# Performance work log

Hardware: AMD Instinct MI355X
Metric: run time of the kernel (lower is better)

## Reference

```python
import jax, jax.numpy as jnp
import numpy as np
from jax import lax

B, T, V, D, K = 64, 512, 32000, 768, 29

def setup_inputs() -> dict:
    key = jax.random.key(0)
    ks = jax.random.split(key, 8)
    x = jax.random.randint(ks[0], (B, T), 0, V)
    tags = jax.random.randint(ks[1], (B, T), 0, K)
    emb = jax.random.normal(ks[2], (V, D), dtype=jnp.float32) * 0.02
    w = jax.random.normal(ks[3], (K, D), dtype=jnp.float32) * 0.02
    b = jnp.zeros((K,), dtype=jnp.float32)
    start_trans = jax.random.normal(ks[4], (K,), dtype=jnp.float32) * 0.1
    end_trans = jax.random.normal(ks[5], (K,), dtype=jnp.float32) * 0.1
    trans = jax.random.normal(ks[6], (K, K), dtype=jnp.float32) * 0.1
    return {"x": x, "tags": tags, "emb": emb, "w": w, "b": b,
            "start_trans": start_trans, "end_trans": end_trans, "trans": trans}

def _emissions(x, emb, w, b):
    e = emb[x]                                   # [B,T,D] (dropout is identity at inference)
    return jnp.einsum('btd,kd->btk', e, w) + b   # [B,T,K]

def _crf_nll(em, tags, start_trans, end_trans, trans):
    # numerator: score of the gold tag path (full mask)
    num = start_trans[tags[:, 0]]
    num = num + jnp.take_along_axis(em[:, 0], tags[:, 0:1], axis=1)[:, 0]
    num = num + jnp.sum(trans[tags[:, :-1], tags[:, 1:]], axis=1)
    num = num + jnp.sum(jnp.take_along_axis(em[:, 1:], tags[:, 1:, None], axis=2)[..., 0], axis=1)
    num = num + end_trans[tags[:, -1]]
    # denominator: forward algorithm (log partition)
    def step(alpha, e_t):
        # alpha [B,K] prev-tag scores; e_t [B,K] current emissions
        nxt = jax.nn.logsumexp(alpha[:, :, None] + trans[None], axis=1) + e_t
        return nxt, None
    alpha0 = start_trans[None] + em[:, 0]
    alpha, _ = lax.scan(step, alpha0, jnp.swapaxes(em[:, 1:], 0, 1))
    logZ = jax.nn.logsumexp(alpha + end_trans[None], axis=1)
    return -jnp.sum(num - logZ)  # torchcrf default reduction='sum', model negates

def _viterbi(em, start_trans, end_trans, trans):
    def vstep(score, e_t):
        cand = score[:, :, None] + trans[None]   # [B,K_prev,K_cur]
        bp = jnp.argmax(cand, axis=1)            # [B,K]
        return jnp.max(cand, axis=1) + e_t, bp
    score0 = start_trans[None] + em[:, 0]
    score, bps = lax.scan(vstep, score0, jnp.swapaxes(em[:, 1:], 0, 1))  # bps [T-1,B,K]
    last = jnp.argmax(score + end_trans[None], axis=1)                   # [B]
    def back(tag, bp):
        prev = jnp.take_along_axis(bp, tag[:, None], axis=1)[:, 0]
        return prev, prev
    _, path = lax.scan(back, last, bps, reverse=True)                    # [T-1,B], tags 0..T-2
    return jnp.concatenate([jnp.swapaxes(path, 0, 1), last[:, None]], axis=1)

def reference(x, tags, emb, w, b, start_trans, end_trans, trans):
    em = _emissions(x, emb, w, b)
    nll = _crf_nll(em, tags, start_trans, end_trans, trans)
    decoded = _viterbi(em, start_trans, end_trans, trans)
    return nll, decoded
```

## Files before the change

kernel.cpp:

```cpp
#include <hip/hip_runtime.h>
#include <math.h>

#define NB 64
#define NT 512
#define ND 768
#define NK 29
#define L2E 1.4426950408889634f
#define LN2 0.6931471805599453f
#define NEG_BIG -1e30f

typedef __attribute__((ext_vector_type(8))) short short8;
typedef __attribute__((ext_vector_type(4))) float floatx4;

__device__ __forceinline__ short bf16r(float f) {
    unsigned u = __float_as_uint(f);
    unsigned r = (u + 0x7FFFu + ((u >> 16) & 1u)) >> 16;
    return (short)r;
}

__device__ __forceinline__ float rlane(float v, int i) {
    return __int_as_float(__builtin_amdgcn_readlane(__float_as_int(v), i));
}

__global__ __launch_bounds__(256) void k_prep(const float* __restrict__ w,
                                              short* __restrict__ wbf)
{
    int i = blockIdx.x * 256 + threadIdx.x;
    if (i < 32 * ND) {
        int row = i / ND;
        wbf[i] = (row < NK) ? bf16r(w[i]) : (short)0;
    }
}

__global__ __launch_bounds__(128) void k_emissions(
    const int* __restrict__ x, const float* __restrict__ emb,
    const short* __restrict__ wbf, const float* __restrict__ bias,
    float* __restrict__ em)
{
    __shared__ float red[2 * 256];
    const int lane = threadIdx.x & 63;
    const int wv = threadIdx.x >> 6;
    const int col = lane & 15;
    const int quad = lane >> 4;
    const int Mbase = blockIdx.x * 16;
    const int tok = Mbase + col;

    const float* arow = emb + (size_t)x[tok] * ND + wv * 384 + quad * 8;
    const short* brow0 = wbf + (size_t)col * ND + wv * 384 + quad * 8;
    const short* brow1 = brow0 + 16 * ND;

    float4 a[24];
#pragma unroll
    for (int c = 0; c < 12; ++c) {
        a[2 * c]     = *(const float4*)(arow + c * 32);
        a[2 * c + 1] = *(const float4*)(arow + c * 32 + 4);
    }

    floatx4 acc0 = {0.f, 0.f, 0.f, 0.f};
    floatx4 acc1 = {0.f, 0.f, 0.f, 0.f};

    short8 b0 = *(const short8*)(brow0);
    short8 b1 = *(const short8*)(brow1);

#pragma unroll
    for (int c = 0; c < 12; ++c) {
        int c1 = (c + 1 <= 11) ? c + 1 : 11;
        short8 nb0 = *(const short8*)(brow0 + c1 * 32);
        short8 nb1 = *(const short8*)(brow1 + c1 * 32);

        short8 af;
        af[0] = bf16r(a[2 * c].x);     af[1] = bf16r(a[2 * c].y);
        af[2] = bf16r(a[2 * c].z);     af[3] = bf16r(a[2 * c].w);
        af[4] = bf16r(a[2 * c + 1].x); af[5] = bf16r(a[2 * c + 1].y);
        af[6] = bf16r(a[2 * c + 1].z); af[7] = bf16r(a[2 * c + 1].w);

        acc0 = __builtin_amdgcn_mfma_f32_16x16x32_bf16(af, b0, acc0, 0, 0, 0);
        acc1 = __builtin_amdgcn_mfma_f32_16x16x32_bf16(af, b1, acc1, 0, 0, 0);

        b0 = nb0; b1 = nb1;
    }

    const int r0 = quad * 4;
    if (wv == 1) {
#pragma unroll
        for (int reg = 0; reg < 4; ++reg) {
            red[(r0 + reg) * 16 + col]       = acc0[reg];
            red[256 + (r0 + reg) * 16 + col] = acc1[reg];
        }
    }
    __syncthreads();
    if (wv == 0) {
        float bs0 = bias[col];
        float bs1 = (col < NK - 16) ? bias[16 + col] : 0.f;
#pragma unroll
        for (int reg = 0; reg < 4; ++reg) {
            int row = r0 + reg;
            float v0 = acc0[reg] + red[row * 16 + col] + bs0;
            em[(size_t)(Mbase + row) * NK + col] = v0;
            if (col < NK - 16) {
                float v1 = acc1[reg] + red[256 + row * 16 + col] + bs1;
                em[(size_t)(Mbase + row) * NK + 16 + col] = v1;
            }
        }
    }
}

__global__ __launch_bounds__(64) void k_scan(
    const float* __restrict__ em, const int* __restrict__ tags,
    const float* __restrict__ st, const float* __restrict__ en,
    const float* __restrict__ tr, float* __restrict__ part,
    float* __restrict__ out)
{
    __shared__ __align__(16) unsigned char smem[NT * NK * 4];
    const int lane = threadIdx.x;
    const int c = lane & 31;
    const int jc = (c < NK) ? c : NK - 1;

    if (blockIdx.x < NB) {
        const int b = blockIdx.x;
        float* emS = (float*)smem;
        {
            const float4* src = (const float4*)(em + (size_t)b * NT * NK);
            float4* dst = (float4*)emS;
            for (int i = lane; i < NT * NK / 4; i += 64) dst[i] = src[i];
        }
        float EC[32];
#pragma unroll
        for (int i = 0; i < NK; ++i) EC[i] = __expf(tr[i * NK + jc]);
#pragma unroll
        for (int i = NK; i < 32; ++i) EC[i] = 0.f;

        float anew = __expf(st[jc] + emS[jc]);

        int eshift = 5 * (NT - 1);
        float eemc = exp2f(fmaf(emS[NK + jc], L2E, -5.0f));
        float rawn = emS[2 * NK + jc];

        for (int t = 1; t < NT; ++t) {
            float curm = (c < NK) ? anew : 0.f;
            float S[32];
#pragma unroll
            for (int i = 0; i < 32; ++i) S[i] = rlane(curm, i);
            float p0 = 0.f, p1 = 0.f, p2 = 0.f, p3 = 0.f;
#pragma unroll
            for (int ii = 0; ii < 8; ++ii) {
                p0 = fmaf(S[4 * ii + 0], EC[4 * ii + 0], p0);
                p1 = fmaf(S[4 * ii + 1], EC[4 * ii + 1], p1);
                p2 = fmaf(S[4 * ii + 2], EC[4 * ii + 2], p2);
                p3 = fmaf(S[4 * ii + 3], EC[4 * ii + 3], p3);
            }
            anew = ((p0 + p1) + (p2 + p3)) * eemc;
            eemc = exp2f(fmaf(rawn, L2E, -5.0f));
            int tn = t + 2; tn = tn < NT ? tn : NT - 1;
            rawn = emS[tn * NK + jc];

            if ((t & 15) == 0) {
                unsigned mb = (unsigned)__builtin_amdgcn_readfirstlane(
                                  __float_as_int(anew));
                int ex = (int)((mb >> 23) & 255u) - 127;
                anew *= __int_as_float((unsigned)(127 - ex) << 23);
                eshift += ex;
            }
        }
        float val = (lane < NK) ? anew * __expf(en[jc]) : 0.f;
#pragma unroll
        for (int s = 32; s; s >>= 1) val += __shfl_xor(val, s);
        float logZ = logf(val) + (float)eshift * LN2;
        const int* tg = tags + b * NT;
        float p = 0.f;
        for (int t = lane; t < NT; t += 64) {
            int tt = tg[t];
            p += emS[t * NK + tt];
            if (t == 0) p += st[tt];
            else        p += tr[tg[t - 1] * NK + tt];
            if (t == NT - 1) p += en[tt];
        }
#pragma unroll
        for (int s = 32; s; s >>= 1) p += __shfl_xor(p, s);
        if (lane == 0) part[b] = logZ - p;
    } else {
        const int b = blockIdx.x - NB;
        const float* emb_b = em + (size_t)b * NT * NK;
        unsigned char* sbp = smem;
        unsigned char* smap = smem + 511 * 32;

        float Tc[32];
#pragma unroll
        for (int i = 0; i < NK; ++i) Tc[i] = tr[i * NK + jc];
#pragma unroll
        for (int i = NK; i < 32; ++i) Tc[i] = 0.f;

        float sc = (c < NK) ? (st[jc] + emb_b[jc]) : NEG_BIG;

        float e0 = emb_b[1 * NK + jc];
        float e1 = emb_b[2 * NK + jc];
        float e2 = emb_b[3 * NK + jc];
        float e3 = emb_b[4 * NK + jc];

        auto vstep = [&](int t, float emt) {
            float S[32];
#pragma unroll
            for (int i = 0; i < 32; ++i) S[i] = rlane(sc, i);
            float v[32]; int id[32];
#pragma unroll
            for (int i = 0; i < 32; ++i) { v[i] = S[i] + Tc[i]; id[i] = i; }
#pragma unroll
            for (int w2 = 16; w2 >= 1; w2 >>= 1)
#pragma unroll
                for (int i = 0; i < 16; ++i) {
                    if (i < w2) {
                        bool g = v[i + w2] > v[i];
                        v[i] = g ? v[i + w2] : v[i];
                        id[i] = g ? id[i + w2] : id[i];
                    }
                }
            if (lane < 32) sbp[(t - 1) * 32 + lane] = (unsigned char)id[0];
            sc = (c < NK) ? (v[0] + emt) : NEG_BIG;
        };

        int t = 1;
        for (; t + 3 < NT; t += 4) {
            vstep(t + 0, e0); { int tn = t + 4; tn = tn < NT ? tn : NT - 1; e0 = emb_b[tn * NK + jc]; }
            vstep(t + 1, e1); { int tn = t + 5; tn = tn < NT ? tn : NT - 1; e1 = emb_b[tn * NK + jc]; }
            vstep(t + 2, e2); { int tn = t + 6; tn = tn < NT ? tn : NT - 1; e2 = emb_b[tn * NK + jc]; }
            vstep(t + 3, e3); { int tn = t + 7; tn = tn < NT ? tn : NT - 1; e3 = emb_b[tn * NK + jc]; }
        }
        vstep(509, e0); vstep(510, e1); vstep(511, e2);

        float vfin = (lane < NK) ? (sc + en[jc]) : NEG_BIG;
        float M = vfin;
#pragma unroll
        for (int s = 32; s; s >>= 1) M = fmaxf(M, __shfl_xor(M, s));
        unsigned long long mk = __ballot((lane < NK) && vfin == M);
        int last = (int)__builtin_ctzll(mk);

        const int h = lane >> 5;
        int cur8[8];
#pragma unroll
        for (int rep = 0; rep < 8; ++rep) cur8[rep] = c;
        for (int off = 0; off < 32; ++off) {
#pragma unroll
            for (int rep = 0; rep < 8; ++rep) {
                int s = 2 * rep + h;
                int hi = (s == 15) ? 511 : 32 * s + 32;
                int r = hi - 1 - off;
                if (r >= 32 * s) cur8[rep] = sbp[r * 32 + cur8[rep]];
            }
        }
#pragma unroll
        for (int rep = 0; rep < 8; ++rep)
            smap[(2 * rep + h) * 32 + c] = (unsigned char)cur8[rep];

        int myhi = 0, cur = last;
        for (int s = 15; s >= 0; --s) {
            if (lane == s) myhi = cur;
            cur = smap[s * 32 + cur];
        }
        float* op = out + 1 + (size_t)b * NT;
        if (lane == 16) op[NT - 1] = (float)last;
        if (lane < 16) {
            int s = lane;
            int hi = (s == 15) ? 511 : 32 * s + 32;
            int cc = myhi;
            for (int r = hi - 1; r >= 32 * s; --r) {
                cc = sbp[r * 32 + cc];
                op[r] = (float)cc;
            }
        }
    }
}

__global__ __launch_bounds__(64) void k_finish(const float* __restrict__ part,
                                               float* __restrict__ out)
{
    float v = part[threadIdx.x];
#pragma unroll
    for (int s = 32; s; s >>= 1) v += __shfl_xor(v, s);
    if (threadIdx.x == 0) out[0] = v;
}

extern "C" void kernel_launch(void* const* d_in, const int* in_sizes, int n_in,
                              void* d_out, int out_size, void* d_ws, size_t ws_size,
                              hipStream_t stream) {
    const int*   x    = (const int*)d_in[0];
    const int*   tags = (const int*)d_in[1];
    const float* emb  = (const float*)d_in[2];
    const float* w    = (const float*)d_in[3];
    const float* bias = (const float*)d_in[4];
    const float* st   = (const float*)d_in[5];
    const float* en   = (const float*)d_in[6];
    const float* tr   = (const float*)d_in[7];
    float* out = (float*)d_out;

    short* wbf  = (short*)d_ws;
    float* part = (float*)((char*)d_ws + 49152);
    float* em   = (float*)((char*)d_ws + 65536);

    k_prep<<<96, 256, 0, stream>>>(w, wbf);
    k_emissions<<<2048, 128, 0, stream>>>(x, emb, wbf, bias, em);
    k_scan<<<2 * NB, 64, 0, stream>>>(em, tags, st, en, tr, part, out);
    k_finish<<<1, 64, 0, stream>>>(part, out);
}
```

Before: 343.1 us.

## Interleave multiple sequences per wavefront in CRF forward and Viterbi scans

Each forward-algorithm wavefront now handles four batch sequences and each Viterbi wavefront handles two, interleaving their independent recurrences so their latency chains overlap. The per-step broadcast of the state vector moves from 32 readlane ops to an LDS store followed by float4 LDS loads. Emissions are read straight from global memory instead of being staged into LDS first. In exchange, fewer blocks are launched (48 instead of 128), each running a longer serial loop, which lowers parallelism across the GPU.

```diff
diff --git a/kernel.cpp b/kernel.cpp
--- a/kernel.cpp
+++ b/kernel.cpp
@@ -5,6 +5,7 @@
 #define NT 512
 #define ND 768
 #define NK 29
+#define NCRF 16
 #define L2E 1.4426950408889634f
 #define LN2 0.6931471805599453f
 #define NEG_BIG -1e30f
@@ -16,10 +17,6 @@
     unsigned u = __float_as_uint(f);
     unsigned r = (u + 0x7FFFu + ((u >> 16) & 1u)) >> 16;
     return (short)r;
-}
-
-__device__ __forceinline__ float rlane(float v, int i) {
-    return __int_as_float(__builtin_amdgcn_readlane(__float_as_int(v), i));
 }
 
 __global__ __launch_bounds__(256) void k_prep(const float* __restrict__ w,
@@ -111,18 +108,19 @@
     const float* __restrict__ tr, float* __restrict__ part,
     float* __restrict__ out)
 {
-    __shared__ __align__(16) unsigned char smem[NT * NK * 4];
+    __shared__ __align__(16) float sAll[4 * 32];
+    __shared__ __align__(16) unsigned char smem[2 * 511 * 32 + 512];
     const int lane = threadIdx.x;
-    const int c = lane & 31;
-    const int jc = (c < NK) ? c : NK - 1;
-
-    if (blockIdx.x < NB) {
-        const int b = blockIdx.x;
-        float* emS = (float*)smem;
-        {
-            const float4* src = (const float4*)(em + (size_t)b * NT * NK);
-            float4* dst = (float4*)emS;
-            for (int i = lane; i < NT * NK / 4; i += 64) dst[i] = src[i];
+    const int jc = (lane < NK) ? lane : NK - 1;
+
+    if (blockIdx.x < NCRF) {
+        const int bI = blockIdx.x;
+        const float* emk[4];
+        const int* tgk[4];
+#pragma unroll
+        for (int k = 0; k < 4; ++k) {
+            emk[k] = em + (size_t)(4 * bI + k) * NT * NK;
+            tgk[k] = tags + (size_t)(4 * bI + k) * NT;
         }
         float EC[32];
 #pragma unroll
@@ -130,59 +128,87 @@
 #pragma unroll
         for (int i = NK; i < 32; ++i) EC[i] = 0.f;
 
-        float anew = __expf(st[jc] + emS[jc]);
-
-        int eshift = 5 * (NT - 1);
-        float eemc = exp2f(fmaf(emS[NK + jc], L2E, -5.0f));
-        float rawn = emS[2 * NK + jc];
+        float anew[4], eemc[4], rawn[4];
+        int eshift[4];
+#pragma unroll
+        for (int k = 0; k < 4; ++k) {
+            anew[k] = __expf(st[jc] + emk[k][jc]);
+            if (lane < 32) sAll[32 * k + lane] = (lane < NK) ? anew[k] : 0.f;
+            eshift[k] = 5 * (NT - 1);
+            eemc[k] = exp2f(fmaf(emk[k][NK + jc], L2E, -5.0f));
+            rawn[k] = emk[k][2 * NK + jc];
+        }
 
         for (int t = 1; t < NT; ++t) {
-            float curm = (c < NK) ? anew : 0.f;
-            float S[32];
-#pragma unroll
-            for (int i = 0; i < 32; ++i) S[i] = rlane(curm, i);
-            float p0 = 0.f, p1 = 0.f, p2 = 0.f, p3 = 0.f;
-#pragma unroll
-            for (int ii = 0; ii < 8; ++ii) {
-                p0 = fmaf(S[4 * ii + 0], EC[4 * ii + 0], p0);
-                p1 = fmaf(S[4 * ii + 1], EC[4 * ii + 1], p1);
-                p2 = fmaf(S[4 * ii + 2], EC[4 * ii + 2], p2);
-                p3 = fmaf(S[4 * ii + 3], EC[4 * ii + 3], p3);
-            }
-            anew = ((p0 + p1) + (p2 + p3)) * eemc;
-            eemc = exp2f(fmaf(rawn, L2E, -5.0f));
-            int tn = t + 2; tn = tn < NT ? tn : NT - 1;
-            rawn = emS[tn * NK + jc];
-
+#pragma unroll
+            for (int k = 0; k < 4; ++k) {
+                const float4* sA4 = (const float4*)(sAll + 32 * k);
+                float4 A[8];
+#pragma unroll
+                for (int ii = 0; ii < 8; ++ii) A[ii] = sA4[ii];
+                float p0 = 0.f, p1 = 0.f, p2 = 0.f, p3 = 0.f;
+#pragma unroll
+                for (int ii = 0; ii < 8; ++ii) {
+                    p0 = fmaf(A[ii].x, EC[4 * ii + 0], p0);
+                    p1 = fmaf(A[ii].y, EC[4 * ii + 1], p1);
+                    p2 = fmaf(A[ii].z, EC[4 * ii + 2], p2);
+                    p3 = fmaf(A[ii].w, EC[4 * ii + 3], p3);
+                }
+                anew[k] = ((p0 + p1) + (p2 + p3)) * eemc[k];
+                eemc[k] = exp2f(fmaf(rawn[k], L2E, -5.0f));
+                int tn = t + 2; tn = tn < NT ? tn : NT - 1;
+                rawn[k] = emk[k][tn * NK + jc];
+            }
             if ((t & 15) == 0) {
-                unsigned mb = (unsigned)__builtin_amdgcn_readfirstlane(
-                                  __float_as_int(anew));
-                int ex = (int)((mb >> 23) & 255u) - 127;
-                anew *= __int_as_float((unsigned)(127 - ex) << 23);
-                eshift += ex;
-            }
-        }
-        float val = (lane < NK) ? anew * __expf(en[jc]) : 0.f;
-#pragma unroll
-        for (int s = 32; s; s >>= 1) val += __shfl_xor(val, s);
-        float logZ = logf(val) + (float)eshift * LN2;
-        const int* tg = tags + b * NT;
-        float p = 0.f;
-        for (int t = lane; t < NT; t += 64) {
-            int tt = tg[t];
-            p += emS[t * NK + tt];
-            if (t == 0) p += st[tt];
-            else        p += tr[tg[t - 1] * NK + tt];
-            if (t == NT - 1) p += en[tt];
-        }
-#pragma unroll
-        for (int s = 32; s; s >>= 1) p += __shfl_xor(p, s);
-        if (lane == 0) part[b] = logZ - p;
+#pragma unroll
+                for (int k = 0; k < 4; ++k) {
+                    unsigned mb = (unsigned)__builtin_amdgcn_readfirstlane(
+                                      __float_as_int(anew[k]));
+                    int ex = (int)((mb >> 23) & 255u) - 127;
+                    anew[k] *= __int_as_float((unsigned)(127 - ex) << 23);
+                    eshift[k] += ex;
+                }
+            }
+#pragma unroll
+            for (int k = 0; k < 4; ++k)
+                if (lane < 32) sAll[32 * k + lane] = (lane < NK) ? anew[k] : 0.f;
+        }
+
+        float pp[4] = {0.f, 0.f, 0.f, 0.f};
+#pragma unroll
+        for (int it = 0; it < 8; ++it) {
+            int t = lane + 64 * it;
+#pragma unroll
+            for (int k = 0; k < 4; ++k) {
+                int tt = tgk[k][t];
+                pp[k] += emk[k][t * NK + tt];
+                if (t == 0) pp[k] += st[tt];
+                else        pp[k] += tr[tgk[k][t - 1] * NK + tt];
+                if (t == NT - 1) pp[k] += en[tt];
+            }
+        }
+#pragma unroll
+        for (int k = 0; k < 4; ++k) {
+            float val = (lane < NK) ? anew[k] * __expf(en[jc]) : 0.f;
+#pragma unroll
+            for (int s = 32; s; s >>= 1) val += __shfl_xor(val, s);
+            float logZ = logf(val) + (float)eshift[k] * LN2;
+            float p = pp[k];
+#pragma unroll
+            for (int s = 32; s; s >>= 1) p += __shfl_xor(p, s);
+            if (lane == 0) part[4 * bI + k] = logZ - p;
+        }
     } else {
-        const int b = blockIdx.x - NB;
-        const float* emb_b = em + (size_t)b * NT * NK;
-        unsigned char* sbp = smem;
-        unsigned char* smap = smem + 511 * 32;
+        const int b0 = 2 * (blockIdx.x - NCRF);
+        const float* emA = em + (size_t)b0 * NT * NK;
+        const float* emB = emA + NT * NK;
+        unsigned char* sbpA = smem;
+        unsigned char* sbpB = smem + 511 * 32;
+        unsigned char* smap = smem + 2 * 511 * 32;
+        float* sA_A = sAll;
+        float* sA_B = sAll + 32;
+        const float4* sA_A4 = (const float4*)sA_A;
+        const float4* sA_B4 = (const float4*)sA_B;
 
         float Tc[32];
 #pragma unroll
@@ -190,81 +216,141 @@
 #pragma unroll
         for (int i = NK; i < 32; ++i) Tc[i] = 0.f;
 
-        float sc = (c < NK) ? (st[jc] + emb_b[jc]) : NEG_BIG;
-
-        float e0 = emb_b[1 * NK + jc];
-        float e1 = emb_b[2 * NK + jc];
-        float e2 = emb_b[3 * NK + jc];
-        float e3 = emb_b[4 * NK + jc];
-
-        auto vstep = [&](int t, float emt) {
-            float S[32];
-#pragma unroll
-            for (int i = 0; i < 32; ++i) S[i] = rlane(sc, i);
-            float v[32]; int id[32];
-#pragma unroll
-            for (int i = 0; i < 32; ++i) { v[i] = S[i] + Tc[i]; id[i] = i; }
-#pragma unroll
-            for (int w2 = 16; w2 >= 1; w2 >>= 1)
-#pragma unroll
-                for (int i = 0; i < 16; ++i) {
-                    if (i < w2) {
+        float scA = (lane < NK) ? (st[jc] + emA[jc]) : NEG_BIG;
+        float scB = (lane < NK) ? (st[jc] + emB[jc]) : NEG_BIG;
+        if (lane < 32) {
+            sA_A[lane] = (lane < NK) ? scA : NEG_BIG;
+            sA_B[lane] = (lane < NK) ? scB : NEG_BIG;
+        }
+
+        float eA0 = emA[1 * NK + jc], eA1 = emA[2 * NK + jc];
+        float eA2 = emA[3 * NK + jc], eA3 = emA[4 * NK + jc];
+        float eB0 = emB[1 * NK + jc], eB1 = emB[2 * NK + jc];
+        float eB2 = emB[3 * NK + jc], eB3 = emB[4 * NK + jc];
+
+        auto vstep2 = [&](int t, float emtA, float emtB) {
+            float4 qA[8], qB[8];
+#pragma unroll
+            for (int ii = 0; ii < 8; ++ii) qA[ii] = sA_A4[ii];
+#pragma unroll
+            for (int ii = 0; ii < 8; ++ii) qB[ii] = sA_B4[ii];
+            {
+                float v[32]; int id[32];
+#pragma unroll
+                for (int ii = 0; ii < 8; ++ii) {
+                    v[4 * ii + 0] = qA[ii].x + Tc[4 * ii + 0];
+                    v[4 * ii + 1] = qA[ii].y + Tc[4 * ii + 1];
+                    v[4 * ii + 2] = qA[ii].z + Tc[4 * ii + 2];
+                    v[4 * ii + 3] = qA[ii].w + Tc[4 * ii + 3];
+                }
+#pragma unroll
+                for (int i = 0; i < 32; ++i) id[i] = i;
+#pragma unroll
+                for (int w2 = 16; w2 >= 1; w2 >>= 1)
+#pragma unroll
+                    for (int i = 0; i < 16; ++i) if (i < w2) {
                         bool g = v[i + w2] > v[i];
                         v[i] = g ? v[i + w2] : v[i];
                         id[i] = g ? id[i + w2] : id[i];
                     }
-                }
-            if (lane < 32) sbp[(t - 1) * 32 + lane] = (unsigned char)id[0];
-            sc = (c < NK) ? (v[0] + emt) : NEG_BIG;
+                if (lane < 32) sbpA[(t - 1) * 32 + lane] = (unsigned char)id[0];
+                scA = (lane < NK) ? (v[0] + emtA) : NEG_BIG;
+                if (lane < 32) sA_A[lane] = (lane < NK) ? scA : NEG_BIG;
+            }
+            {
+                float v[32]; int id[32];
+#pragma unroll
+                for (int ii = 0; ii < 8; ++ii) {
+                    v[4 * ii + 0] = qB[ii].x + Tc[4 * ii + 0];
+                    v[4 * ii + 1] = qB[ii].y + Tc[4 * ii + 1];
+                    v[4 * ii + 2] = qB[ii].z + Tc[4 * ii + 2];
+                    v[4 * ii + 3] = qB[ii].w + Tc[4 * ii + 3];
+                }
+#pragma unroll
+                for (int i = 0; i < 32; ++i) id[i] = i;
+#pragma unroll
+                for (int w2 = 16; w2 >= 1; w2 >>= 1)
+#pragma unroll
+                    for (int i = 0; i < 16; ++i) if (i < w2) {
+                        bool g = v[i + w2] > v[i];
+                        v[i] = g ? v[i + w2] : v[i];
+                        id[i] = g ? id[i + w2] : id[i];
+                    }
+                if (lane < 32) sbpB[(t - 1) * 32 + lane] = (unsigned char)id[0];
+                scB = (lane < NK) ? (v[0] + emtB) : NEG_BIG;
+                if (lane < 32) sA_B[lane] = (lane < NK) ? scB : NEG_BIG;
+            }
         };
 
         int t = 1;
         for (; t + 3 < NT; t += 4) {
-            vstep(t + 0, e0); { int tn = t + 4; tn = tn < NT ? tn : NT - 1; e0 = emb_b[tn * NK + jc]; }
-            vstep(t + 1, e1); { int tn = t + 5; tn = tn < NT ? tn : NT - 1; e1 = emb_b[tn * NK + jc]; }
-            vstep(t + 2, e2); { int tn = t + 6; tn = tn < NT ? tn : NT - 1; e2 = emb_b[tn * NK + jc]; }
-            vstep(t + 3, e3); { int tn = t + 7; tn = tn < NT ? tn : NT - 1; e3 = emb_b[tn * NK + jc]; }
-        }
-        vstep(509, e0); vstep(510, e1); vstep(511, e2);
-
-        float vfin = (lane < NK) ? (sc + en[jc]) : NEG_BIG;
-        float M = vfin;
-#pragma unroll
-        for (int s = 32; s; s >>= 1) M = fmaxf(M, __shfl_xor(M, s));
-        unsigned long long mk = __ballot((lane < NK) && vfin == M);
-        int last = (int)__builtin_ctzll(mk);
-
+            vstep2(t + 0, eA0, eB0);
+            { int tn = t + 4; tn = tn < NT ? tn : NT - 1;
+              eA0 = emA[tn * NK + jc]; eB0 = emB[tn * NK + jc]; }
+            vstep2(t + 1, eA1, eB1);
+            { int tn = t + 5; tn = tn < NT ? tn : NT - 1;
+              eA1 = emA[tn * NK + jc]; eB1 = emB[tn * NK + jc]; }
+            vstep2(t + 2, eA2, eB2);
+            { int tn = t + 6; tn = tn < NT ? tn : NT - 1;
+              eA2 = emA[tn * NK + jc]; eB2 = emB[tn * NK + jc]; }
+            vstep2(t + 3, eA3, eB3);
+            { int tn = t + 7; tn = tn < NT ? tn : NT - 1;
+              eA3 = emA[tn * NK + jc]; eB3 = emB[tn * NK + jc]; }
+        }
+        vstep2(509, eA0, eB0); vstep2(510, eA1, eB1); vstep2(511, eA2, eB2);
+
+        float vfA = (lane < NK) ? (scA + en[jc]) : NEG_BIG;
+        float MA = vfA;
+#pragma unroll
+        for (int s = 32; s; s >>= 1) MA = fmaxf(MA, __shfl_xor(MA, s));
+        unsigned long long mkA = __ballot((lane < NK) && vfA == MA);
+        int lastA = (int)__builtin_ctzll(mkA);
+
+        float vfB = (lane < NK) ? (scB + en[jc]) : NEG_BIG;
+        float MB = vfB;
+#pragma unroll
+        for (int s = 32; s; s >>= 1) MB = fmaxf(MB, __shfl_xor(MB, s));
+        unsigned long long mkB = __ballot((lane < NK) && vfB == MB);
+        int lastB = (int)__builtin_ctzll(mkB);
+
+        const int c = lane & 31;
         const int h = lane >> 5;
-        int cur8[8];
-#pragma unroll
-        for (int rep = 0; rep < 8; ++rep) cur8[rep] = c;
-        for (int off = 0; off < 32; ++off) {
-#pragma unroll
-            for (int rep = 0; rep < 8; ++rep) {
-                int s = 2 * rep + h;
+#pragma unroll
+        for (int chain = 0; chain < 2; ++chain) {
+            const unsigned char* sbp = chain ? sbpB : sbpA;
+            int last = chain ? lastB : lastA;
+            float* op = out + 1 + (size_t)(b0 + chain) * NT;
+
+            int cur8[8];
+#pragma unroll
+            for (int rep = 0; rep < 8; ++rep) cur8[rep] = c;
+            for (int off = 0; off < 32; ++off) {
+#pragma unroll
+                for (int rep = 0; rep < 8; ++rep) {
+                    int s = 2 * rep + h;
+                    int hi = (s == 15) ? 511 : 32 * s + 32;
+                    int r = hi - 1 - off;
+                    if (r >= 32 * s) cur8[rep] = sbp[r * 32 + cur8[rep]];
+                }
+            }
+#pragma unroll
+            for (int rep = 0; rep < 8; ++rep)
+                smap[(2 * rep + h) * 32 + c] = (unsigned char)cur8[rep];
+
+            int myhi = 0, cur = last;
+            for (int s = 15; s >= 0; --s) {
+                if (lane == s) myhi = cur;
+                cur = smap[s * 32 + cur];
+            }
+            if (lane == 16) op[NT - 1] = (float)last;
+            if (lane < 16) {
+                int s = lane;
                 int hi = (s == 15) ? 511 : 32 * s + 32;
-                int r = hi - 1 - off;
-                if (r >= 32 * s) cur8[rep] = sbp[r * 32 + cur8[rep]];
-            }
-        }
-#pragma unroll
-        for (int rep = 0; rep < 8; ++rep)
-            smap[(2 * rep + h) * 32 + c] = (unsigned char)cur8[rep];
-
-        int myhi = 0, cur = last;
-        for (int s = 15; s >= 0; --s) {
-            if (lane == s) myhi = cur;
-            cur = smap[s * 32 + cur];
-        }
-        float* op = out + 1 + (size_t)b * NT;
-        if (lane == 16) op[NT - 1] = (float)last;
-        if (lane < 16) {
-            int s = lane;
-            int hi = (s == 15) ? 511 : 32 * s + 32;
-            int cc = myhi;
-            for (int r = hi - 1; r >= 32 * s; --r) {
-                cc = sbp[r * 32 + cc];
-                op[r] = (float)cc;
+                int cc = myhi;
+                for (int r = hi - 1; r >= 32 * s; --r) {
+                    cc = sbp[r * 32 + cc];
+                    op[r] = (float)cc;
+                }
             }
         }
     }
@@ -298,6 +384,6 @@
 
     k_prep<<<96, 256, 0, stream>>>(w, wbf);
     k_emissions<<<2048, 128, 0, stream>>>(x, emb, wbf, bias, em);
-    k_scan<<<2 * NB, 64, 0, stream>>>(em, tags, st, en, tr, part, out);
+    k_scan<<<NCRF + NB / 2, 64, 0, stream>>>(em, tags, st, en, tr, part, out);
     k_finish<<<1, 64, 0, stream>>>(part, out);
 }
```

After: 567.5 us. 65.4% more time.

## Split Viterbi argmax out of serial scan into parallel backpointer kernel

Applied to the files above, without the earlier changes.

The serial Viterbi scan now does only a max reduction per step and writes every step's score vector to global memory. A new kernel with 512 threads per batch row recomputes the argmax backpointers for all time steps in parallel from the stored scores, then runs the backtrace. Both scans also broadcast state through shared memory with float4 reads instead of 32 readlanes. This takes the argmax index tracking off the serial dependency chain, at the cost of an extra launch, global traffic for the states, and per-step LDS round trips in a single wave.

```diff
diff --git a/kernel.cpp b/kernel.cpp
--- a/kernel.cpp
+++ b/kernel.cpp
@@ -18,10 +18,6 @@
     return (short)r;
 }
 
-__device__ __forceinline__ float rlane(float v, int i) {
-    return __int_as_float(__builtin_amdgcn_readlane(__float_as_int(v), i));
-}
-
 __global__ __launch_bounds__(256) void k_prep(const float* __restrict__ w,
                                               short* __restrict__ wbf)
 {
@@ -109,12 +105,13 @@
     const float* __restrict__ em, const int* __restrict__ tags,
     const float* __restrict__ st, const float* __restrict__ en,
     const float* __restrict__ tr, float* __restrict__ part,
-    float* __restrict__ out)
-{
+    float* __restrict__ states)
+{
+    __shared__ __align__(16) float sA[32];
     __shared__ __align__(16) unsigned char smem[NT * NK * 4];
+    const float4* sA4 = (const float4*)sA;
     const int lane = threadIdx.x;
-    const int c = lane & 31;
-    const int jc = (c < NK) ? c : NK - 1;
+    const int jc = (lane < NK) ? lane : NK - 1;
 
     if (blockIdx.x < NB) {
         const int b = blockIdx.x;
@@ -130,24 +127,25 @@
 #pragma unroll
         for (int i = NK; i < 32; ++i) EC[i] = 0.f;
 
-        float anew = __expf(st[jc] + emS[jc]);
+        float a0v = __expf(st[jc] + emS[jc]);
+        if (lane < 32) sA[lane] = (lane < NK) ? a0v : 0.f;
 
         int eshift = 5 * (NT - 1);
         float eemc = exp2f(fmaf(emS[NK + jc], L2E, -5.0f));
         float rawn = emS[2 * NK + jc];
+        float anew = a0v;
 
         for (int t = 1; t < NT; ++t) {
-            float curm = (c < NK) ? anew : 0.f;
-            float S[32];
-#pragma unroll
-            for (int i = 0; i < 32; ++i) S[i] = rlane(curm, i);
+            float4 A[8];
+#pragma unroll
+            for (int ii = 0; ii < 8; ++ii) A[ii] = sA4[ii];
             float p0 = 0.f, p1 = 0.f, p2 = 0.f, p3 = 0.f;
 #pragma unroll
             for (int ii = 0; ii < 8; ++ii) {
-                p0 = fmaf(S[4 * ii + 0], EC[4 * ii + 0], p0);
-                p1 = fmaf(S[4 * ii + 1], EC[4 * ii + 1], p1);
-                p2 = fmaf(S[4 * ii + 2], EC[4 * ii + 2], p2);
-                p3 = fmaf(S[4 * ii + 3], EC[4 * ii + 3], p3);
+                p0 = fmaf(A[ii].x, EC[4 * ii + 0], p0);
+                p1 = fmaf(A[ii].y, EC[4 * ii + 1], p1);
+                p2 = fmaf(A[ii].z, EC[4 * ii + 2], p2);
+                p3 = fmaf(A[ii].w, EC[4 * ii + 3], p3);
             }
             anew = ((p0 + p1) + (p2 + p3)) * eemc;
             eemc = exp2f(fmaf(rawn, L2E, -5.0f));
@@ -161,6 +159,7 @@
                 anew *= __int_as_float((unsigned)(127 - ex) << 23);
                 eshift += ex;
             }
+            if (lane < 32) sA[lane] = (lane < NK) ? anew : 0.f;
         }
         float val = (lane < NK) ? anew * __expf(en[jc]) : 0.f;
 #pragma unroll
@@ -181,8 +180,7 @@
     } else {
         const int b = blockIdx.x - NB;
         const float* emb_b = em + (size_t)b * NT * NK;
-        unsigned char* sbp = smem;
-        unsigned char* smap = smem + 511 * 32;
+        float* stt = states + (size_t)b * NT * 32;
 
         float Tc[32];
 #pragma unroll
@@ -190,7 +188,8 @@
 #pragma unroll
         for (int i = NK; i < 32; ++i) Tc[i] = 0.f;
 
-        float sc = (c < NK) ? (st[jc] + emb_b[jc]) : NEG_BIG;
+        float sc = (lane < NK) ? (st[jc] + emb_b[jc]) : NEG_BIG;
+        if (lane < 32) { sA[lane] = sc; stt[lane] = sc; }
 
         float e0 = emb_b[1 * NK + jc];
         float e1 = emb_b[2 * NK + jc];
@@ -198,24 +197,36 @@
         float e3 = emb_b[4 * NK + jc];
 
         auto vstep = [&](int t, float emt) {
-            float S[32];
-#pragma unroll
-            for (int i = 0; i < 32; ++i) S[i] = rlane(sc, i);
-            float v[32]; int id[32];
-#pragma unroll
-            for (int i = 0; i < 32; ++i) { v[i] = S[i] + Tc[i]; id[i] = i; }
-#pragma unroll
-            for (int w2 = 16; w2 >= 1; w2 >>= 1)
-#pragma unroll
-                for (int i = 0; i < 16; ++i) {
-                    if (i < w2) {
-                        bool g = v[i + w2] > v[i];
-                        v[i] = g ? v[i + w2] : v[i];
-                        id[i] = g ? id[i + w2] : id[i];
-                    }
-                }
-            if (lane < 32) sbp[(t - 1) * 32 + lane] = (unsigned char)id[0];
-            sc = (c < NK) ? (v[0] + emt) : NEG_BIG;
+            float4 q[8];
+#pragma unroll
+            for (int ii = 0; ii < 8; ++ii) q[ii] = sA4[ii];
+            float v[32];
+#pragma unroll
+            for (int ii = 0; ii < 8; ++ii) {
+                v[4 * ii + 0] = q[ii].x + Tc[4 * ii + 0];
+                v[4 * ii + 1] = q[ii].y + Tc[4 * ii + 1];
+                v[4 * ii + 2] = q[ii].z + Tc[4 * ii + 2];
+                v[4 * ii + 3] = q[ii].w + Tc[4 * ii + 3];
+            }
+            float w0 = fmaxf(fmaxf(v[0], v[1]), v[2]);
+            float w1 = fmaxf(fmaxf(v[3], v[4]), v[5]);
+            float w2 = fmaxf(fmaxf(v[6], v[7]), v[8]);
+            float w3 = fmaxf(fmaxf(v[9], v[10]), v[11]);
+            float w4 = fmaxf(fmaxf(v[12], v[13]), v[14]);
+            float w5 = fmaxf(fmaxf(v[15], v[16]), v[17]);
+            float w6 = fmaxf(fmaxf(v[18], v[19]), v[20]);
+            float w7 = fmaxf(fmaxf(v[21], v[22]), v[23]);
+            float w8 = fmaxf(fmaxf(v[24], v[25]), v[26]);
+            float w9 = fmaxf(fmaxf(v[27], v[28]), v[29]);
+            float wa = fmaxf(v[30], v[31]);
+            float u0 = fmaxf(fmaxf(w0, w1), w2);
+            float u1 = fmaxf(fmaxf(w3, w4), w5);
+            float u2 = fmaxf(fmaxf(w6, w7), w8);
+            float u3 = fmaxf(w9, wa);
+            float m  = fmaxf(fmaxf(fmaxf(u0, u1), u2), u3);
+
+            sc = (lane < NK) ? (m + emt) : NEG_BIG;
+            if (lane < 32) { sA[lane] = sc; stt[t * 32 + lane] = sc; }
         };
 
         int t = 1;
@@ -226,18 +237,82 @@
             vstep(t + 3, e3); { int tn = t + 7; tn = tn < NT ? tn : NT - 1; e3 = emb_b[tn * NK + jc]; }
         }
         vstep(509, e0); vstep(510, e1); vstep(511, e2);
-
-        float vfin = (lane < NK) ? (sc + en[jc]) : NEG_BIG;
+    }
+}
+
+__global__ __launch_bounds__(512) void k_bp(
+    const float* __restrict__ states, const float* __restrict__ en,
+    const float* __restrict__ tr, float* __restrict__ out)
+{
+    __shared__ __align__(16) float stt[256 * 32];
+    __shared__ unsigned char sbp[511 * 32];
+    __shared__ unsigned char smap[16 * 32];
+    const int b = blockIdx.x;
+    const float* S = states + (size_t)b * NT * 32;
+    const int tid = threadIdx.x;
+    const int c = tid & 31;
+    const int jc = (c < NK) ? c : NK - 1;
+    const int g = tid >> 5;
+
+    float Tc[32];
+#pragma unroll
+    for (int i = 0; i < NK; ++i) Tc[i] = tr[i * NK + jc];
+#pragma unroll
+    for (int i = NK; i < 32; ++i) Tc[i] = 0.f;
+
+    for (int half = 0; half < 2; ++half) {
+        __syncthreads();
+        {
+            const float4* src = (const float4*)(S + half * 256 * 32);
+            float4* dst = (float4*)stt;
+#pragma unroll
+            for (int i = 0; i < 4; ++i) dst[tid + 512 * i] = src[tid + 512 * i];
+        }
+        __syncthreads();
+#pragma unroll 1
+        for (int k = 0; k < 16; ++k) {
+            int t = 256 * half + 1 + g + 16 * k;
+            if (t < NT) {
+                const float4* row = (const float4*)(stt + (t - 1 - 256 * half) * 32);
+                float v[32]; int id[32];
+#pragma unroll
+                for (int ii = 0; ii < 8; ++ii) {
+                    float4 q = row[ii];
+                    v[4 * ii + 0] = q.x + Tc[4 * ii + 0];
+                    v[4 * ii + 1] = q.y + Tc[4 * ii + 1];
+                    v[4 * ii + 2] = q.z + Tc[4 * ii + 2];
+                    v[4 * ii + 3] = q.w + Tc[4 * ii + 3];
+                }
+#pragma unroll
+                for (int i = 0; i < 32; ++i) id[i] = i;
+#pragma unroll
+                for (int w2 = 16; w2 >= 1; w2 >>= 1)
+#pragma unroll
+                    for (int i = 0; i < 16; ++i) if (i < w2) {
+                        bool gg = v[i + w2] > v[i];
+                        v[i] = gg ? v[i + w2] : v[i];
+                        id[i] = gg ? id[i + w2] : id[i];
+                    }
+                sbp[(t - 1) * 32 + c] = (unsigned char)id[0];
+            }
+        }
+    }
+    __syncthreads();
+
+    if (tid < 64) {
+        const int lane = tid;
+        float vfin = (lane < NK) ? (stt[255 * 32 + lane] + en[jc]) : NEG_BIG;
         float M = vfin;
 #pragma unroll
         for (int s = 32; s; s >>= 1) M = fmaxf(M, __shfl_xor(M, s));
         unsigned long long mk = __ballot((lane < NK) && vfin == M);
         int last = (int)__builtin_ctzll(mk);
 
+        const int cl = lane & 31;
         const int h = lane >> 5;
         int cur8[8];
 #pragma unroll
-        for (int rep = 0; rep < 8; ++rep) cur8[rep] = c;
+        for (int rep = 0; rep < 8; ++rep) cur8[rep] = cl;
         for (int off = 0; off < 32; ++off) {
 #pragma unroll
             for (int rep = 0; rep < 8; ++rep) {
@@ -249,7 +324,7 @@
         }
 #pragma unroll
         for (int rep = 0; rep < 8; ++rep)
-            smap[(2 * rep + h) * 32 + c] = (unsigned char)cur8[rep];
+            smap[(2 * rep + h) * 32 + cl] = (unsigned char)cur8[rep];
 
         int myhi = 0, cur = last;
         for (int s = 15; s >= 0; --s) {
@@ -292,12 +367,14 @@
     const float* tr   = (const float*)d_in[7];
     float* out = (float*)d_out;
 
-    short* wbf  = (short*)d_ws;
-    float* part = (float*)((char*)d_ws + 49152);
-    float* em   = (float*)((char*)d_ws + 65536);
+    short* wbf    = (short*)d_ws;
+    float* part   = (float*)((char*)d_ws + 49152);
+    float* em     = (float*)((char*)d_ws + 65536);
+    float* states = (float*)((char*)d_ws + 3932160);
 
     k_prep<<<96, 256, 0, stream>>>(w, wbf);
     k_emissions<<<2048, 128, 0, stream>>>(x, emb, wbf, bias, em);
-    k_scan<<<2 * NB, 64, 0, stream>>>(em, tags, st, en, tr, part, out);
+    k_scan<<<2 * NB, 64, 0, stream>>>(em, tags, st, en, tr, part, states);
+    k_bp<<<NB, 512, 0, stream>>>(states, en, tr, out);
     k_finish<<<1, 64, 0, stream>>>(part, out);
 }
```

New measurement: 510.0 us. 1.49x slower.
